# Kernel optimization log

Hardware: AMD Instinct MI355X
Metric: run time of the kernel (lower is better)

The kernel has to match this reference:

```python
import jax, jax.numpy as jnp
import numpy as np

NUM_EXPERTS = 8
M_TOTAL = 16384      # total routed tokens, sorted by expert
IN_FEATURES = 2048
OUT_FEATURES = 2048


def setup_inputs() -> dict:
    key = jax.random.key(0)
    k1, k2 = jax.random.split(key)
    x = jax.random.normal(k1, (M_TOTAL, IN_FEATURES), dtype=jnp.float32)
    # moe_fused_kaiming_uniform_: uniform(-sqrt(3*5/in), +sqrt(3*5/in))
    bound = float(np.sqrt(3.0 * 5.0 / IN_FEATURES))
    weight = jax.random.uniform(
        k2, (NUM_EXPERTS, OUT_FEATURES, IN_FEATURES),
        dtype=jnp.float32, minval=-bound, maxval=bound)
    # variable-size expert groups that sum exactly to M_TOTAL
    rng = np.random.default_rng(0)
    cuts = np.sort(rng.choice(np.arange(1, M_TOTAL), NUM_EXPERTS - 1, replace=False))
    m_sizes = np.diff(np.concatenate([[0], cuts, [M_TOTAL]])).astype(np.int32)
    return {"input": x, "weight": weight, "m_sizes": jnp.asarray(m_sizes)}


def reference(input, weight, m_sizes):
    """Grouped GEMM: rows of `input` are sorted by expert; the e-th contiguous
    block of m_sizes[e] rows is multiplied by weight[e].T ([out, in] -> x @ W_e^T)."""
    num_experts, out_features, _ = weight.shape
    m = input.shape[0]
    # per-token expert id from group sizes (jit-safe: fixed total length)
    expert_ids = jnp.repeat(jnp.arange(num_experts, dtype=jnp.int32), m_sizes,
                            total_repeat_length=m)  # [M]
    out = jnp.zeros((m, out_features), dtype=input.dtype)
    for e in range(num_experts):  # small fixed expert count
        mask = (expert_ids == e)[:, None]
        out = out + jnp.where(mask, input @ weight[e].T, jnp.zeros((), input.dtype))
    return out
```

## Files before the change

### kernel.cpp

```cpp
#include <hip/hip_runtime.h>
#include <hip/hip_bf16.h>

#define M_TOTAL 16384
#define KDIM 2048
#define NDIM 2048
#define NEXP 8
#define BM 256
#define BN 256
#define BK 32
#define NKT 64
#define MAX_ROW_TILES 71
#define NWG (MAX_ROW_TILES * 8)

typedef __attribute__((ext_vector_type(8))) __bf16 bf16x8;
typedef __attribute__((ext_vector_type(4))) float f32x4;

__device__ inline int minI(int a, int b) { return a < b ? a : b; }

__device__ inline bf16x8 cvt8(float4 a, float4 b) {
  bf16x8 r;
  r[0] = (__bf16)a.x; r[1] = (__bf16)a.y; r[2] = (__bf16)a.z; r[3] = (__bf16)a.w;
  r[4] = (__bf16)b.x; r[5] = (__bf16)b.y; r[6] = (__bf16)b.z; r[7] = (__bf16)b.w;
  return r;
}

__device__ inline void gload16(const void* g, void* l) {
  __builtin_amdgcn_global_load_lds(
      (const __attribute__((address_space(1))) void*)g,
      (__attribute__((address_space(3))) void*)l, 16, 0, 0);
}

__global__ __launch_bounds__(256) void cvt_both(
    const float* __restrict__ x, const float* __restrict__ w,
    bf16x8* __restrict__ xb, bf16x8* __restrict__ wb) {
  const int NX = (M_TOTAL * KDIM) / 8;
  const int NW = (NEXP * NDIM * KDIM) / 8;
  const int stride = gridDim.x * blockDim.x;
  for (int i = blockIdx.x * blockDim.x + threadIdx.x; i < NX + NW; i += stride) {
    const float4* src = (i < NX) ? ((const float4*)x + (size_t)i * 2)
                                 : ((const float4*)w + (size_t)(i - NX) * 2);
    float4 a = src[0], b = src[1];
    bf16x8 c = cvt8(a, b);
    if (i < NX) xb[i] = c; else wb[i - NX] = c;
  }
}

__global__ __launch_bounds__(512, 2) void moe_gemm_pipe(
    const __hip_bfloat16* __restrict__ xb, const __hip_bfloat16* __restrict__ wb,
    const int* __restrict__ ms, float* __restrict__ out) {
  __shared__ __align__(16) char lds[131072];

  const int orig = blockIdx.x;
  const int wg = (orig & 7) * MAX_ROW_TILES + (orig >> 3);
  const int bt = wg >> 3;
  const int ntile = wg & 7;

  int sizes[NEXP];
#pragma unroll
  for (int i = 0; i < NEXP; ++i) sizes[i] = ms[i];
  int e = 0, row0 = 0, rows = 0, acc_t = 0, start = 0;
  bool found = false;
#pragma unroll
  for (int i = 0; i < NEXP; ++i) {
    int nt = (sizes[i] + BM - 1) >> 8;
    if (!found && bt < acc_t + nt) {
      found = true; e = i;
      int tt = bt - acc_t;
      row0 = start + tt * BM;
      rows = minI(sizes[i] - tt * BM, BM);
    }
    acc_t += nt; start += sizes[i];
  }
  if (!found) return;

  const int tid = threadIdx.x;
  const int lane = tid & 63;
  const int wave = tid >> 6;
  const int wr = wave >> 2, wc = wave & 3;
  const int col0 = ntile * BN;

  const int rwh = wave * 16 + (lane >> 2);
  const int colel = (((lane & 3) ^ ((lane >> 3) & 3)) << 3);
  const __hip_bfloat16* aS0 = xb + (size_t)minI(row0 + rwh, M_TOTAL - 1) * KDIM + colel;
  const __hip_bfloat16* aS1 = xb + (size_t)minI(row0 + 128 + rwh, M_TOTAL - 1) * KDIM + colel;
  const __hip_bfloat16* wbase = wb + (size_t)e * NDIM * KDIM;
  const __hip_bfloat16* bS0 = wbase + (size_t)(col0 + rwh) * KDIM + colel;
  const __hip_bfloat16* bS1 = wbase + (size_t)(col0 + 128 + rwh) * KDIM + colel;
  char* stBase = lds + wave * 1024;

  const int fr = lane & 15, fc = lane >> 4;
  const int laneOff = fr * 64 + ((fc ^ ((fr >> 1) & 3)) << 4);
  const int aOff = wr * 8192 + laneOff;
  const int bOff = 16384 + wc * 4096 + laneOff;

  f32x4 acc[8][4];
  const f32x4 zero = {0.f, 0.f, 0.f, 0.f};
#pragma unroll
  for (int i = 0; i < 8; ++i)
#pragma unroll
    for (int j = 0; j < 4; ++j) acc[i][j] = zero;

  bf16x8 afL0[4], afL1[4], bv0[4], bv1[4], afH[4];

#define ISSUE_A(T) { char* b_ = stBase + ((T) & 3) * 32768; \
    gload16(aS0 + (size_t)(T) * BK, b_); gload16(aS1 + (size_t)(T) * BK, b_ + 8192); }
#define ISSUE_B(T) { char* b_ = stBase + ((T) & 3) * 32768 + 16384; \
    gload16(bS0 + (size_t)(T) * BK, b_); gload16(bS1 + (size_t)(T) * BK, b_ + 8192); }
#define DS_AFH(T) { const char* bA_ = lds + ((T) & 3) * 32768 + aOff + 4096; \
    _Pragma("unroll") for (int mt = 0; mt < 4; ++mt) \
      afH[mt] = *(const bf16x8*)(bA_ + mt * 1024); }
#define DS_NEXT(T, S) { const char* bb_ = lds + ((T) & 3) * 32768; \
    _Pragma("unroll") for (int mt = 0; mt < 4; ++mt) \
      afL##S[mt] = *(const bf16x8*)(bb_ + aOff + mt * 1024); \
    _Pragma("unroll") for (int nt = 0; nt < 4; ++nt) \
      bv##S[nt] = *(const bf16x8*)(bb_ + bOff + nt * 1024); }
#define MFMA_P0(S) { _Pragma("unroll") for (int mt = 0; mt < 4; ++mt) \
    _Pragma("unroll") for (int nt = 0; nt < 4; ++nt) \
      acc[mt][nt] = __builtin_amdgcn_mfma_f32_16x16x32_bf16( \
          afL##S[mt], bv##S[nt], acc[mt][nt], 0, 0, 0); }
#define MFMA_P1(S) { _Pragma("unroll") for (int mt = 0; mt < 4; ++mt) \
    _Pragma("unroll") for (int nt = 0; nt < 4; ++nt) \
      acc[mt + 4][nt] = __builtin_amdgcn_mfma_f32_16x16x32_bf16( \
          afH[mt], bv##S[nt], acc[mt + 4][nt], 0, 0, 0); }

#define TILE(T, S, SN, IA, IB, VMNSTR, NF) { \
    DS_AFH(T); \
    if (IA) ISSUE_A((T) + 3); \
    __builtin_amdgcn_s_setprio(1); MFMA_P0(S); __builtin_amdgcn_s_setprio(0); \
    asm volatile("s_waitcnt " VMNSTR ::: "memory"); \
    __builtin_amdgcn_s_barrier(); \
    if (NF) DS_NEXT((T) + 1, SN); \
    if (IB) ISSUE_B((T) + 3); \
    __builtin_amdgcn_s_setprio(1); MFMA_P1(S); __builtin_amdgcn_s_setprio(0); }

  ISSUE_A(0) ISSUE_B(0) ISSUE_A(1) ISSUE_B(1) ISSUE_A(2) ISSUE_B(2)
  asm volatile("s_waitcnt vmcnt(8)" ::: "memory");
  __builtin_amdgcn_s_barrier();
  DS_NEXT(0, 0);

  for (int tp = 0; tp < 30; ++tp) {
    const int t = tp * 2;
    TILE(t,     0, 1, true, true, "vmcnt(6)", true);
    TILE(t + 1, 1, 0, true, true, "vmcnt(6)", true);
  }
  TILE(60, 0, 1, true,  true,  "vmcnt(6)", true);
  TILE(61, 1, 0, false, false, "vmcnt(4)", true);
  TILE(62, 0, 1, false, false, "vmcnt(0)", true);
  TILE(63, 1, 0, false, false, "vmcnt(0)", false);

#undef TILE
#undef MFMA_P1
#undef MFMA_P0
#undef DS_NEXT
#undef DS_AFH
#undef ISSUE_B
#undef ISSUE_A

  const int er = (lane >> 4) * 4;
#pragma unroll
  for (int mt = 0; mt < 8; ++mt) {
#pragma unroll
    for (int j = 0; j < 4; ++j) {
      int r = wr * 128 + mt * 16 + er + j;
      if (r < rows) {
        float* op = out + (size_t)(row0 + r) * NDIM + col0 + wc * 64 + (lane & 15);
#pragma unroll
        for (int nt = 0; nt < 4; ++nt) op[nt * 16] = acc[mt][nt][j];
      }
    }
  }
}

__global__ __launch_bounds__(256) void moe_gemm_f32(
    const float* __restrict__ x, const float* __restrict__ w,
    const int* __restrict__ ms, float* __restrict__ out) {
  __shared__ __align__(16) char As[128 * 64 * 2];
  __shared__ __align__(16) char Bs[128 * 64 * 2];
  int sizes[NEXP];
#pragma unroll
  for (int i = 0; i < NEXP; ++i) sizes[i] = ms[i];
  const int bt = blockIdx.y;
  int e = 0, row0 = 0, rows = 0, acc_t = 0, start = 0;
  bool found = false;
#pragma unroll
  for (int i = 0; i < NEXP; ++i) {
    int nt = (sizes[i] + 127) >> 7;
    if (!found && bt < acc_t + nt) {
      found = true; e = i;
      int tt = bt - acc_t;
      row0 = start + tt * 128;
      rows = minI(sizes[i] - tt * 128, 128);
    }
    acc_t += nt; start += sizes[i];
  }
  if (!found) return;
  const int tid = threadIdx.x;
  const int lane = tid & 63;
  const int wave = tid >> 6;
  const int wm = wave >> 1, wn = wave & 1;
  const int col0 = blockIdx.x * 128;
  const float* wbase = w + (size_t)e * (size_t)NDIM * KDIM;
  const int sr = tid >> 1;
  const int sh = tid & 1;
  const float* aptr = x + (size_t)(row0 + sr) * KDIM + sh * 32;
  const float* bptr = wbase + (size_t)(col0 + sr) * KDIM + sh * 32;
  const bool aval = (sr < rows);
  f32x4 acc[4][4];
  const f32x4 zero = {0.f, 0.f, 0.f, 0.f};
#pragma unroll
  for (int i = 0; i < 4; ++i)
#pragma unroll
    for (int j = 0; j < 4; ++j) acc[i][j] = zero;
  for (int kb = 0; kb < KDIM / 64; ++kb) {
    {
      float4 v[8];
      if (aval) {
        const float4* p = (const float4*)(aptr + kb * 64);
#pragma unroll
        for (int j = 0; j < 8; ++j) v[j] = p[j];
      } else {
#pragma unroll
        for (int j = 0; j < 8; ++j) v[j] = make_float4(0.f, 0.f, 0.f, 0.f);
      }
#pragma unroll
      for (int j = 0; j < 4; ++j) {
        bf16x8 c = cvt8(v[2 * j], v[2 * j + 1]);
        int chunk = (sh * 4 + j) ^ (sr & 7);
        *(bf16x8*)(As + sr * 128 + chunk * 16) = c;
      }
    }
    {
      const float4* p = (const float4*)(bptr + kb * 64);
      float4 u[8];
#pragma unroll
      for (int j = 0; j < 8; ++j) u[j] = p[j];
#pragma unroll
      for (int j = 0; j < 4; ++j) {
        bf16x8 c = cvt8(u[2 * j], u[2 * j + 1]);
        int chunk = (sh * 4 + j) ^ (sr & 7);
        *(bf16x8*)(Bs + sr * 128 + chunk * 16) = c;
      }
    }
    __syncthreads();
#pragma unroll
    for (int ks = 0; ks < 2; ++ks) {
      bf16x8 afr[4], bfv[4];
#pragma unroll
      for (int mt = 0; mt < 4; ++mt) {
        int r = wm * 64 + mt * 16 + (lane & 15);
        int chunk = (ks * 4 + (lane >> 4)) ^ (r & 7);
        afr[mt] = *(const bf16x8*)(As + r * 128 + chunk * 16);
      }
#pragma unroll
      for (int nt = 0; nt < 4; ++nt) {
        int r = wn * 64 + nt * 16 + (lane & 15);
        int chunk = (ks * 4 + (lane >> 4)) ^ (r & 7);
        bfv[nt] = *(const bf16x8*)(Bs + r * 128 + chunk * 16);
      }
#pragma unroll
      for (int mt = 0; mt < 4; ++mt)
#pragma unroll
        for (int nt = 0; nt < 4; ++nt)
          acc[mt][nt] = __builtin_amdgcn_mfma_f32_16x16x32_bf16(
              afr[mt], bfv[nt], acc[mt][nt], 0, 0, 0);
    }
    __syncthreads();
  }
#pragma unroll
  for (int mt = 0; mt < 4; ++mt) {
#pragma unroll
    for (int j = 0; j < 4; ++j) {
      int r = wm * 64 + mt * 16 + (lane >> 4) * 4 + j;
      if (r < rows) {
        float* op = out + (size_t)(row0 + r) * NDIM + col0 + wn * 64 + (lane & 15);
#pragma unroll
        for (int nt = 0; nt < 4; ++nt) op[nt * 16] = acc[mt][nt][j];
      }
    }
  }
}

extern "C" void kernel_launch(void* const* d_in, const int* in_sizes, int n_in,
                              void* d_out, int out_size, void* d_ws, size_t ws_size,
                              hipStream_t stream) {
  const float* x = (const float*)d_in[0];
  const float* w = (const float*)d_in[1];
  const int* ms = (const int*)d_in[2];
  float* out = (float*)d_out;
  const size_t nx = (size_t)M_TOTAL * KDIM;
  const size_t nw = (size_t)NEXP * NDIM * KDIM;
  const size_t need = (nx + nw) * sizeof(__hip_bfloat16);
  if (ws_size >= need) {
    __hip_bfloat16* xb = (__hip_bfloat16*)d_ws;
    __hip_bfloat16* wb = xb + nx;
    cvt_both<<<2048, 256, 0, stream>>>(x, w, (bf16x8*)xb, (bf16x8*)wb);
    moe_gemm_pipe<<<dim3(NWG), dim3(512), 0, stream>>>(xb, wb, ms, out);
  } else {
    moe_gemm_f32<<<dim3(16, 135), dim3(256), 0, stream>>>(x, w, ms, out);
  }
}
```

Baseline: 243.5 us.

## Shrink GEMM tile to 256x128 with 3-stage LDS ring for more occupancy

```diff
diff --git a/kernel.cpp b/kernel.cpp
--- a/kernel.cpp
+++ b/kernel.cpp
@@ -6,11 +6,12 @@
 #define NDIM 2048
 #define NEXP 8
 #define BM 256
-#define BN 256
+#define BN 128
 #define BK 32
-#define NKT 64
-#define MAX_ROW_TILES 71
-#define NWG (MAX_ROW_TILES * 8)
+#define RT_MAX 71
+#define CT 16
+#define NWG (RT_MAX * CT)
+#define BUFB 24576
 
 typedef __attribute__((ext_vector_type(8))) __bf16 bf16x8;
 typedef __attribute__((ext_vector_type(4))) float f32x4;
@@ -45,15 +46,15 @@
   }
 }
 
-__global__ __launch_bounds__(512, 2) void moe_gemm_pipe(
+__global__ __launch_bounds__(512, 4) void moe_gemm_cores(
     const __hip_bfloat16* __restrict__ xb, const __hip_bfloat16* __restrict__ wb,
     const int* __restrict__ ms, float* __restrict__ out) {
-  __shared__ __align__(16) char lds[131072];
+  __shared__ __align__(16) char lds[3 * BUFB];
 
   const int orig = blockIdx.x;
-  const int wg = (orig & 7) * MAX_ROW_TILES + (orig >> 3);
-  const int bt = wg >> 3;
-  const int ntile = wg & 7;
+  const int wg = (orig & 7) * (NWG / 8) + (orig >> 3);
+  const int bt = wg >> 4;
+  const int ntile = wg & 15;
 
   int sizes[NEXP];
 #pragma unroll
@@ -76,7 +77,7 @@
   const int tid = threadIdx.x;
   const int lane = tid & 63;
   const int wave = tid >> 6;
-  const int wr = wave >> 2, wc = wave & 3;
+  const int wr = wave >> 1, wc = wave & 1;
   const int col0 = ntile * BN;
 
   const int rwh = wave * 16 + (lane >> 2);
@@ -84,84 +85,73 @@
   const __hip_bfloat16* aS0 = xb + (size_t)minI(row0 + rwh, M_TOTAL - 1) * KDIM + colel;
   const __hip_bfloat16* aS1 = xb + (size_t)minI(row0 + 128 + rwh, M_TOTAL - 1) * KDIM + colel;
   const __hip_bfloat16* wbase = wb + (size_t)e * NDIM * KDIM;
-  const __hip_bfloat16* bS0 = wbase + (size_t)(col0 + rwh) * KDIM + colel;
-  const __hip_bfloat16* bS1 = wbase + (size_t)(col0 + 128 + rwh) * KDIM + colel;
-  char* stBase = lds + wave * 1024;
+  const __hip_bfloat16* bS = wbase + (size_t)(col0 + rwh) * KDIM + colel;
 
   const int fr = lane & 15, fc = lane >> 4;
-  const int laneOff = fr * 64 + ((fc ^ ((fr >> 1) & 3)) << 4);
-  const int aOff = wr * 8192 + laneOff;
-  const int bOff = 16384 + wc * 4096 + laneOff;
-
-  f32x4 acc[8][4];
+  int offA[4], offB[4];
+#pragma unroll
+  for (int mt = 0; mt < 4; ++mt) {
+    int r = wr * 64 + mt * 16 + fr;
+    offA[mt] = r * 64 + ((fc ^ ((r >> 1) & 3)) << 4);
+  }
+#pragma unroll
+  for (int nt = 0; nt < 4; ++nt) {
+    int r = wc * 64 + nt * 16 + fr;
+    offB[nt] = 16384 + r * 64 + ((fc ^ ((r >> 1) & 3)) << 4);
+  }
+
+  f32x4 acc[4][4];
   const f32x4 zero = {0.f, 0.f, 0.f, 0.f};
 #pragma unroll
-  for (int i = 0; i < 8; ++i)
+  for (int i = 0; i < 4; ++i)
 #pragma unroll
     for (int j = 0; j < 4; ++j) acc[i][j] = zero;
 
-  bf16x8 afL0[4], afL1[4], bv0[4], bv1[4], afH[4];
-
-#define ISSUE_A(T) { char* b_ = stBase + ((T) & 3) * 32768; \
-    gload16(aS0 + (size_t)(T) * BK, b_); gload16(aS1 + (size_t)(T) * BK, b_ + 8192); }
-#define ISSUE_B(T) { char* b_ = stBase + ((T) & 3) * 32768 + 16384; \
-    gload16(bS0 + (size_t)(T) * BK, b_); gload16(bS1 + (size_t)(T) * BK, b_ + 8192); }
-#define DS_AFH(T) { const char* bA_ = lds + ((T) & 3) * 32768 + aOff + 4096; \
+#define ISSUE3(T, BI) { char* b_ = lds + (BI) * BUFB + wave * 1024; \
+    gload16(aS0 + (size_t)(T) * BK, b_); \
+    gload16(aS1 + (size_t)(T) * BK, b_ + 8192); \
+    gload16(bS + (size_t)(T) * BK, b_ + 16384); }
+
+#define TILE(T, BR, BI, VM, DOI) { \
+    asm volatile("s_waitcnt " VM ::: "memory"); \
+    __builtin_amdgcn_s_barrier(); \
+    if (DOI) ISSUE3((T) + 2, BI); \
+    const char* bb_ = lds + (BR) * BUFB; \
+    bf16x8 af[4], bv[4]; \
     _Pragma("unroll") for (int mt = 0; mt < 4; ++mt) \
-      afH[mt] = *(const bf16x8*)(bA_ + mt * 1024); }
-#define DS_NEXT(T, S) { const char* bb_ = lds + ((T) & 3) * 32768; \
+      af[mt] = *(const bf16x8*)(bb_ + offA[mt]); \
+    _Pragma("unroll") for (int nt = 0; nt < 4; ++nt) \
+      bv[nt] = *(const bf16x8*)(bb_ + offB[nt]); \
+    __builtin_amdgcn_s_setprio(1); \
     _Pragma("unroll") for (int mt = 0; mt < 4; ++mt) \
-      afL##S[mt] = *(const bf16x8*)(bb_ + aOff + mt * 1024); \
-    _Pragma("unroll") for (int nt = 0; nt < 4; ++nt) \
-      bv##S[nt] = *(const bf16x8*)(bb_ + bOff + nt * 1024); }
-#define MFMA_P0(S) { _Pragma("unroll") for (int mt = 0; mt < 4; ++mt) \
-    _Pragma("unroll") for (int nt = 0; nt < 4; ++nt) \
-      acc[mt][nt] = __builtin_amdgcn_mfma_f32_16x16x32_bf16( \
-          afL##S[mt], bv##S[nt], acc[mt][nt], 0, 0, 0); }
-#define MFMA_P1(S) { _Pragma("unroll") for (int mt = 0; mt < 4; ++mt) \
-    _Pragma("unroll") for (int nt = 0; nt < 4; ++nt) \
-      acc[mt + 4][nt] = __builtin_amdgcn_mfma_f32_16x16x32_bf16( \
-          afH[mt], bv##S[nt], acc[mt + 4][nt], 0, 0, 0); }
-
-#define TILE(T, S, SN, IA, IB, VMNSTR, NF) { \
-    DS_AFH(T); \
-    if (IA) ISSUE_A((T) + 3); \
-    __builtin_amdgcn_s_setprio(1); MFMA_P0(S); __builtin_amdgcn_s_setprio(0); \
-    asm volatile("s_waitcnt " VMNSTR ::: "memory"); \
-    __builtin_amdgcn_s_barrier(); \
-    if (NF) DS_NEXT((T) + 1, SN); \
-    if (IB) ISSUE_B((T) + 3); \
-    __builtin_amdgcn_s_setprio(1); MFMA_P1(S); __builtin_amdgcn_s_setprio(0); }
-
-  ISSUE_A(0) ISSUE_B(0) ISSUE_A(1) ISSUE_B(1) ISSUE_A(2) ISSUE_B(2)
-  asm volatile("s_waitcnt vmcnt(8)" ::: "memory");
-  __builtin_amdgcn_s_barrier();
-  DS_NEXT(0, 0);
-
-  for (int tp = 0; tp < 30; ++tp) {
-    const int t = tp * 2;
-    TILE(t,     0, 1, true, true, "vmcnt(6)", true);
-    TILE(t + 1, 1, 0, true, true, "vmcnt(6)", true);
-  }
-  TILE(60, 0, 1, true,  true,  "vmcnt(6)", true);
-  TILE(61, 1, 0, false, false, "vmcnt(4)", true);
-  TILE(62, 0, 1, false, false, "vmcnt(0)", true);
-  TILE(63, 1, 0, false, false, "vmcnt(0)", false);
+      _Pragma("unroll") for (int nt = 0; nt < 4; ++nt) \
+        acc[mt][nt] = __builtin_amdgcn_mfma_f32_16x16x32_bf16( \
+            af[mt], bv[nt], acc[mt][nt], 0, 0, 0); \
+    __builtin_amdgcn_s_setprio(0); }
+
+  ISSUE3(0, 0)
+  ISSUE3(1, 1)
+
+  for (int tp = 0; tp < 20; ++tp) {
+    const int t = tp * 3;
+    TILE(t,     0, 2, "vmcnt(3)", true);
+    TILE(t + 1, 1, 0, "vmcnt(3)", true);
+    TILE(t + 2, 2, 1, "vmcnt(3)", true);
+  }
+  TILE(60, 0, 2, "vmcnt(3)", true);
+  TILE(61, 1, 0, "vmcnt(3)", true);
+  TILE(62, 2, 1, "vmcnt(3)", false);
+  TILE(63, 0, 0, "vmcnt(0)", false);
 
 #undef TILE
-#undef MFMA_P1
-#undef MFMA_P0
-#undef DS_NEXT
-#undef DS_AFH
-#undef ISSUE_B
-#undef ISSUE_A
+#undef ISSUE3
 
   const int er = (lane >> 4) * 4;
 #pragma unroll
-  for (int mt = 0; mt < 8; ++mt) {
+  for (int mt = 0; mt < 4; ++mt) {
 #pragma unroll
     for (int j = 0; j < 4; ++j) {
-      int r = wr * 128 + mt * 16 + er + j;
+      int r = wr * 64 + mt * 16 + er + j;
       if (r < rows) {
         float* op = out + (size_t)(row0 + r) * NDIM + col0 + wc * 64 + (lane & 15);
 #pragma unroll
@@ -294,7 +284,7 @@
     __hip_bfloat16* xb = (__hip_bfloat16*)d_ws;
     __hip_bfloat16* wb = xb + nx;
     cvt_both<<<2048, 256, 0, stream>>>(x, w, (bf16x8*)xb, (bf16x8*)wb);
-    moe_gemm_pipe<<<dim3(NWG), dim3(512), 0, stream>>>(xb, wb, ms, out);
+    moe_gemm_cores<<<dim3(NWG), dim3(512), 0, stream>>>(xb, wb, ms, out);
   } else {
     moe_gemm_f32<<<dim3(16, 135), dim3(256), 0, stream>>>(x, w, ms, out);
   }
```

Measured after the change: 256.4 us. 5.3% more time.

## Restructure GEMM main loop into 8-phase double-buffered BK=64 pipeline

Applied to the files above, without the earlier changes.

```diff
diff --git a/kernel.cpp b/kernel.cpp
--- a/kernel.cpp
+++ b/kernel.cpp
@@ -7,8 +7,7 @@
 #define NEXP 8
 #define BM 256
 #define BN 256
-#define BK 32
-#define NKT 64
+#define BK 64
 #define MAX_ROW_TILES 71
 #define NWG (MAX_ROW_TILES * 8)
 
@@ -45,7 +44,7 @@
   }
 }
 
-__global__ __launch_bounds__(512, 2) void moe_gemm_pipe(
+__global__ __launch_bounds__(512, 2) void moe_gemm_8p(
     const __hip_bfloat16* __restrict__ xb, const __hip_bfloat16* __restrict__ wb,
     const int* __restrict__ ms, float* __restrict__ out) {
   __shared__ __align__(16) char lds[131072];
@@ -79,19 +78,23 @@
   const int wr = wave >> 2, wc = wave & 3;
   const int col0 = ntile * BN;
 
-  const int rwh = wave * 16 + (lane >> 2);
-  const int colel = (((lane & 3) ^ ((lane >> 3) & 3)) << 3);
-  const __hip_bfloat16* aS0 = xb + (size_t)minI(row0 + rwh, M_TOTAL - 1) * KDIM + colel;
-  const __hip_bfloat16* aS1 = xb + (size_t)minI(row0 + 128 + rwh, M_TOTAL - 1) * KDIM + colel;
+  const int urow = tid >> 3;
+  const int colel = (((tid & 7) ^ ((tid >> 3) & 7)) << 3);
   const __hip_bfloat16* wbase = wb + (size_t)e * NDIM * KDIM;
-  const __hip_bfloat16* bS0 = wbase + (size_t)(col0 + rwh) * KDIM + colel;
-  const __hip_bfloat16* bS1 = wbase + (size_t)(col0 + 128 + rwh) * KDIM + colel;
-  char* stBase = lds + wave * 1024;
+  const __hip_bfloat16* aP00 = xb + (size_t)minI(row0 +   0 + urow, M_TOTAL - 1) * KDIM + colel;
+  const __hip_bfloat16* aP01 = xb + (size_t)minI(row0 +  64 + urow, M_TOTAL - 1) * KDIM + colel;
+  const __hip_bfloat16* aP10 = xb + (size_t)minI(row0 + 128 + urow, M_TOTAL - 1) * KDIM + colel;
+  const __hip_bfloat16* aP11 = xb + (size_t)minI(row0 + 192 + urow, M_TOTAL - 1) * KDIM + colel;
+  const __hip_bfloat16* bP0 = wbase + (size_t)(col0 +   0 + urow) * KDIM + colel;
+  const __hip_bfloat16* bP1 = wbase + (size_t)(col0 +  64 + urow) * KDIM + colel;
+  const __hip_bfloat16* bP2 = wbase + (size_t)(col0 + 128 + urow) * KDIM + colel;
+  const __hip_bfloat16* bP3 = wbase + (size_t)(col0 + 192 + urow) * KDIM + colel;
 
   const int fr = lane & 15, fc = lane >> 4;
-  const int laneOff = fr * 64 + ((fc ^ ((fr >> 1) & 3)) << 4);
-  const int aOff = wr * 8192 + laneOff;
-  const int bOff = 16384 + wc * 4096 + laneOff;
+  const int swz0 = fr * 128 + (((fc) ^ (fr & 7)) << 4);
+  const int swz1 = fr * 128 + (((4 + fc) ^ (fr & 7)) << 4);
+  const int aBase = wr * 16384;
+  const int bBase = 32768 + (wc >> 1) * 16384 + (wc & 1) * 8192;
 
   f32x4 acc[8][4];
   const f32x4 zero = {0.f, 0.f, 0.f, 0.f};
@@ -100,61 +103,69 @@
 #pragma unroll
     for (int j = 0; j < 4; ++j) acc[i][j] = zero;
 
-  bf16x8 afL0[4], afL1[4], bv0[4], bv1[4], afH[4];
-
-#define ISSUE_A(T) { char* b_ = stBase + ((T) & 3) * 32768; \
-    gload16(aS0 + (size_t)(T) * BK, b_); gload16(aS1 + (size_t)(T) * BK, b_ + 8192); }
-#define ISSUE_B(T) { char* b_ = stBase + ((T) & 3) * 32768 + 16384; \
-    gload16(bS0 + (size_t)(T) * BK, b_); gload16(bS1 + (size_t)(T) * BK, b_ + 8192); }
-#define DS_AFH(T) { const char* bA_ = lds + ((T) & 3) * 32768 + aOff + 4096; \
+  bf16x8 af[4], bv[4];
+
+#define ST_A(D, H, L, KK) gload16(aP##H##L + (size_t)(KK) * BK, \
+    lds + (D) * 65536 + ((H) * 2 + (L)) * 8192 + wave * 1024);
+#define ST_B(D, Q, KK) gload16(bP##Q + (size_t)(KK) * BK, \
+    lds + (D) * 65536 + 32768 + (Q) * 8192 + wave * 1024);
+#define VM4 asm volatile("s_waitcnt vmcnt(4)" ::: "memory");
+#define VM2 asm volatile("s_waitcnt vmcnt(2)" ::: "memory");
+#define VM0 asm volatile("s_waitcnt vmcnt(0)" ::: "memory");
+
+#define PHASE(D, MH, SWZ, LOADB, STAGEBLK, WAITBLK) { \
     _Pragma("unroll") for (int mt = 0; mt < 4; ++mt) \
-      afH[mt] = *(const bf16x8*)(bA_ + mt * 1024); }
-#define DS_NEXT(T, S) { const char* bb_ = lds + ((T) & 3) * 32768; \
+      af[mt] = *(const bf16x8*)(lds + (D) * 65536 + aBase + ((MH) * 4 + mt) * 2048 + SWZ); \
+    if (LOADB) { _Pragma("unroll") for (int nt = 0; nt < 4; ++nt) \
+      bv[nt] = *(const bf16x8*)(lds + (D) * 65536 + bBase + nt * 2048 + SWZ); } \
+    STAGEBLK \
+    __builtin_amdgcn_s_barrier(); \
+    asm volatile("s_waitcnt lgkmcnt(0)" ::: "memory"); \
+    __builtin_amdgcn_s_setprio(1); \
     _Pragma("unroll") for (int mt = 0; mt < 4; ++mt) \
-      afL##S[mt] = *(const bf16x8*)(bb_ + aOff + mt * 1024); \
-    _Pragma("unroll") for (int nt = 0; nt < 4; ++nt) \
-      bv##S[nt] = *(const bf16x8*)(bb_ + bOff + nt * 1024); }
-#define MFMA_P0(S) { _Pragma("unroll") for (int mt = 0; mt < 4; ++mt) \
-    _Pragma("unroll") for (int nt = 0; nt < 4; ++nt) \
-      acc[mt][nt] = __builtin_amdgcn_mfma_f32_16x16x32_bf16( \
-          afL##S[mt], bv##S[nt], acc[mt][nt], 0, 0, 0); }
-#define MFMA_P1(S) { _Pragma("unroll") for (int mt = 0; mt < 4; ++mt) \
-    _Pragma("unroll") for (int nt = 0; nt < 4; ++nt) \
-      acc[mt + 4][nt] = __builtin_amdgcn_mfma_f32_16x16x32_bf16( \
-          afH[mt], bv##S[nt], acc[mt + 4][nt], 0, 0, 0); }
-
-#define TILE(T, S, SN, IA, IB, VMNSTR, NF) { \
-    DS_AFH(T); \
-    if (IA) ISSUE_A((T) + 3); \
-    __builtin_amdgcn_s_setprio(1); MFMA_P0(S); __builtin_amdgcn_s_setprio(0); \
-    asm volatile("s_waitcnt " VMNSTR ::: "memory"); \
+      _Pragma("unroll") for (int nt = 0; nt < 4; ++nt) \
+        acc[(MH) * 4 + mt][nt] = __builtin_amdgcn_mfma_f32_16x16x32_bf16( \
+            af[mt], bv[nt], acc[(MH) * 4 + mt][nt], 0, 0, 0); \
+    __builtin_amdgcn_s_setprio(0); \
+    WAITBLK \
+    asm volatile("" ::: "memory"); \
     __builtin_amdgcn_s_barrier(); \
-    if (NF) DS_NEXT((T) + 1, SN); \
-    if (IB) ISSUE_B((T) + 3); \
-    __builtin_amdgcn_s_setprio(1); MFMA_P1(S); __builtin_amdgcn_s_setprio(0); }
-
-  ISSUE_A(0) ISSUE_B(0) ISSUE_A(1) ISSUE_B(1) ISSUE_A(2) ISSUE_B(2)
-  asm volatile("s_waitcnt vmcnt(8)" ::: "memory");
+    asm volatile("" ::: "memory"); \
+  }
+
+  ST_B(0, 0, 0) ST_B(0, 1, 0) ST_B(0, 2, 0) ST_B(0, 3, 0)
+  ST_A(0, 0, 0, 0) ST_A(0, 1, 0, 0)
+  ST_A(0, 0, 1, 0) ST_A(0, 1, 1, 0)
+  ST_B(1, 0, 1) ST_B(1, 1, 1)
+  VM4
   __builtin_amdgcn_s_barrier();
-  DS_NEXT(0, 0);
-
-  for (int tp = 0; tp < 30; ++tp) {
-    const int t = tp * 2;
-    TILE(t,     0, 1, true, true, "vmcnt(6)", true);
-    TILE(t + 1, 1, 0, true, true, "vmcnt(6)", true);
-  }
-  TILE(60, 0, 1, true,  true,  "vmcnt(6)", true);
-  TILE(61, 1, 0, false, false, "vmcnt(4)", true);
-  TILE(62, 0, 1, false, false, "vmcnt(0)", true);
-  TILE(63, 1, 0, false, false, "vmcnt(0)", false);
-
-#undef TILE
-#undef MFMA_P1
-#undef MFMA_P0
-#undef DS_NEXT
-#undef DS_AFH
-#undef ISSUE_B
-#undef ISSUE_A
+
+  for (int i = 0; i < 15; ++i) {
+    const int t = 2 * i;
+    PHASE(0, 0, swz0, true,  { ST_B(1, 2, t + 1) ST_B(1, 3, t + 1) }, VM4)
+    PHASE(0, 1, swz0, false, { ST_A(1, 0, 0, t + 1) ST_A(1, 1, 0, t + 1) }, )
+    PHASE(0, 0, swz1, true,  { ST_A(1, 0, 1, t + 1) ST_A(1, 1, 1, t + 1) }, )
+    PHASE(0, 1, swz1, false, { ST_B(0, 0, t + 2) ST_B(0, 1, t + 2) }, VM4)
+    PHASE(1, 0, swz0, true,  { ST_B(0, 2, t + 2) ST_B(0, 3, t + 2) }, VM4)
+    PHASE(1, 1, swz0, false, { ST_A(0, 0, 0, t + 2) ST_A(0, 1, 0, t + 2) }, )
+    PHASE(1, 0, swz1, true,  { ST_A(0, 0, 1, t + 2) ST_A(0, 1, 1, t + 2) }, )
+    PHASE(1, 1, swz1, false, { ST_B(1, 0, t + 3) ST_B(1, 1, t + 3) }, VM4)
+  }
+  PHASE(0, 0, swz0, true,  { ST_B(1, 2, 31) ST_B(1, 3, 31) }, VM4)
+  PHASE(0, 1, swz0, false, { ST_A(1, 0, 0, 31) ST_A(1, 1, 0, 31) }, )
+  PHASE(0, 0, swz1, true,  { ST_A(1, 0, 1, 31) ST_A(1, 1, 1, 31) }, )
+  PHASE(0, 1, swz1, false, { }, VM2)
+  PHASE(1, 0, swz0, true,  { }, VM0)
+  PHASE(1, 1, swz0, false, { }, )
+  PHASE(1, 0, swz1, true,  { }, )
+  PHASE(1, 1, swz1, false, { }, )
+
+#undef PHASE
+#undef VM0
+#undef VM2
+#undef VM4
+#undef ST_B
+#undef ST_A
 
   const int er = (lane >> 4) * 4;
 #pragma unroll
@@ -294,7 +305,7 @@
     __hip_bfloat16* xb = (__hip_bfloat16*)d_ws;
     __hip_bfloat16* wb = xb + nx;
     cvt_both<<<2048, 256, 0, stream>>>(x, w, (bf16x8*)xb, (bf16x8*)wb);
-    moe_gemm_pipe<<<dim3(NWG), dim3(512), 0, stream>>>(xb, wb, ms, out);
+    moe_gemm_8p<<<dim3(NWG), dim3(512), 0, stream>>>(xb, wb, ms, out);
   } else {
     moe_gemm_f32<<<dim3(16, 135), dim3(256), 0, stream>>>(x, w, ms, out);
   }
```

Measured after the change: 239.1 us. About the same (-1.8%).

## Replace split-phase register prefetch pipeline with single-barrier 4-stage LDS ring

Applied to the files above, without the earlier changes.

```diff
diff --git a/kernel.cpp b/kernel.cpp
--- a/kernel.cpp
+++ b/kernel.cpp
@@ -8,7 +8,6 @@
 #define BM 256
 #define BN 256
 #define BK 32
-#define NKT 64
 #define MAX_ROW_TILES 71
 #define NWG (MAX_ROW_TILES * 8)
 
@@ -45,7 +44,7 @@
   }
 }
 
-__global__ __launch_bounds__(512, 2) void moe_gemm_pipe(
+__global__ __launch_bounds__(512, 2) void moe_gemm_sb(
     const __hip_bfloat16* __restrict__ xb, const __hip_bfloat16* __restrict__ wb,
     const int* __restrict__ ms, float* __restrict__ out) {
   __shared__ __align__(16) char lds[131072];
@@ -86,12 +85,11 @@
   const __hip_bfloat16* wbase = wb + (size_t)e * NDIM * KDIM;
   const __hip_bfloat16* bS0 = wbase + (size_t)(col0 + rwh) * KDIM + colel;
   const __hip_bfloat16* bS1 = wbase + (size_t)(col0 + 128 + rwh) * KDIM + colel;
-  char* stBase = lds + wave * 1024;
 
   const int fr = lane & 15, fc = lane >> 4;
   const int laneOff = fr * 64 + ((fc ^ ((fr >> 1) & 3)) << 4);
   const int aOff = wr * 8192 + laneOff;
-  const int bOff = 16384 + wc * 4096 + laneOff;
+  const int bOff = 16384 + (wc >> 1) * 8192 + (wc & 1) * 4096 + laneOff;
 
   f32x4 acc[8][4];
   const f32x4 zero = {0.f, 0.f, 0.f, 0.f};
@@ -100,61 +98,52 @@
 #pragma unroll
     for (int j = 0; j < 4; ++j) acc[i][j] = zero;
 
-  bf16x8 afL0[4], afL1[4], bv0[4], bv1[4], afH[4];
-
-#define ISSUE_A(T) { char* b_ = stBase + ((T) & 3) * 32768; \
-    gload16(aS0 + (size_t)(T) * BK, b_); gload16(aS1 + (size_t)(T) * BK, b_ + 8192); }
-#define ISSUE_B(T) { char* b_ = stBase + ((T) & 3) * 32768 + 16384; \
-    gload16(bS0 + (size_t)(T) * BK, b_); gload16(bS1 + (size_t)(T) * BK, b_ + 8192); }
-#define DS_AFH(T) { const char* bA_ = lds + ((T) & 3) * 32768 + aOff + 4096; \
-    _Pragma("unroll") for (int mt = 0; mt < 4; ++mt) \
-      afH[mt] = *(const bf16x8*)(bA_ + mt * 1024); }
-#define DS_NEXT(T, S) { const char* bb_ = lds + ((T) & 3) * 32768; \
-    _Pragma("unroll") for (int mt = 0; mt < 4; ++mt) \
-      afL##S[mt] = *(const bf16x8*)(bb_ + aOff + mt * 1024); \
+#define ST4(BI, T) { char* b_ = lds + (BI) * 32768 + wave * 1024; \
+    gload16(aS0 + (size_t)(T) * BK, b_); \
+    gload16(aS1 + (size_t)(T) * BK, b_ + 8192); \
+    gload16(bS0 + (size_t)(T) * BK, b_ + 16384); \
+    gload16(bS1 + (size_t)(T) * BK, b_ + 24576); }
+#define VM4 "vmcnt(4)"
+#define VM0 "vmcnt(0)"
+
+#define TILE(BI, T, DOST, VM) { \
+    asm volatile("s_waitcnt " VM ::: "memory"); \
+    __builtin_amdgcn_s_barrier(); \
+    asm volatile("" ::: "memory"); \
+    if (DOST) ST4(((BI) + 2) & 3, (T) + 2); \
+    const char* bb_ = lds + (BI) * 32768; \
+    bf16x8 af[8], bv[4]; \
+    _Pragma("unroll") for (int mt = 0; mt < 8; ++mt) \
+      af[mt] = *(const bf16x8*)(bb_ + aOff + mt * 1024); \
     _Pragma("unroll") for (int nt = 0; nt < 4; ++nt) \
-      bv##S[nt] = *(const bf16x8*)(bb_ + bOff + nt * 1024); }
-#define MFMA_P0(S) { _Pragma("unroll") for (int mt = 0; mt < 4; ++mt) \
-    _Pragma("unroll") for (int nt = 0; nt < 4; ++nt) \
-      acc[mt][nt] = __builtin_amdgcn_mfma_f32_16x16x32_bf16( \
-          afL##S[mt], bv##S[nt], acc[mt][nt], 0, 0, 0); }
-#define MFMA_P1(S) { _Pragma("unroll") for (int mt = 0; mt < 4; ++mt) \
-    _Pragma("unroll") for (int nt = 0; nt < 4; ++nt) \
-      acc[mt + 4][nt] = __builtin_amdgcn_mfma_f32_16x16x32_bf16( \
-          afH[mt], bv##S[nt], acc[mt + 4][nt], 0, 0, 0); }
-
-#define TILE(T, S, SN, IA, IB, VMNSTR, NF) { \
-    DS_AFH(T); \
-    if (IA) ISSUE_A((T) + 3); \
-    __builtin_amdgcn_s_setprio(1); MFMA_P0(S); __builtin_amdgcn_s_setprio(0); \
-    asm volatile("s_waitcnt " VMNSTR ::: "memory"); \
-    __builtin_amdgcn_s_barrier(); \
-    if (NF) DS_NEXT((T) + 1, SN); \
-    if (IB) ISSUE_B((T) + 3); \
-    __builtin_amdgcn_s_setprio(1); MFMA_P1(S); __builtin_amdgcn_s_setprio(0); }
-
-  ISSUE_A(0) ISSUE_B(0) ISSUE_A(1) ISSUE_B(1) ISSUE_A(2) ISSUE_B(2)
-  asm volatile("s_waitcnt vmcnt(8)" ::: "memory");
-  __builtin_amdgcn_s_barrier();
-  DS_NEXT(0, 0);
-
-  for (int tp = 0; tp < 30; ++tp) {
-    const int t = tp * 2;
-    TILE(t,     0, 1, true, true, "vmcnt(6)", true);
-    TILE(t + 1, 1, 0, true, true, "vmcnt(6)", true);
-  }
-  TILE(60, 0, 1, true,  true,  "vmcnt(6)", true);
-  TILE(61, 1, 0, false, false, "vmcnt(4)", true);
-  TILE(62, 0, 1, false, false, "vmcnt(0)", true);
-  TILE(63, 1, 0, false, false, "vmcnt(0)", false);
+      bv[nt] = *(const bf16x8*)(bb_ + bOff + nt * 1024); \
+    __builtin_amdgcn_s_setprio(1); \
+    _Pragma("unroll") for (int mt = 0; mt < 8; ++mt) \
+      _Pragma("unroll") for (int nt = 0; nt < 4; ++nt) \
+        acc[mt][nt] = __builtin_amdgcn_mfma_f32_16x16x32_bf16( \
+            af[mt], bv[nt], acc[mt][nt], 0, 0, 0); \
+    __builtin_amdgcn_s_setprio(0); \
+  }
+
+  ST4(0, 0)
+  ST4(1, 1)
+
+  for (int i = 0; i < 15; ++i) {
+    const int t = 4 * i;
+    TILE(0, t,     true, VM4)
+    TILE(1, t + 1, true, VM4)
+    TILE(2, t + 2, true, VM4)
+    TILE(3, t + 3, true, VM4)
+  }
+  TILE(0, 60, true,  VM4)
+  TILE(1, 61, true,  VM4)
+  TILE(2, 62, false, VM4)
+  TILE(3, 63, false, VM0)
 
 #undef TILE
-#undef MFMA_P1
-#undef MFMA_P0
-#undef DS_NEXT
-#undef DS_AFH
-#undef ISSUE_B
-#undef ISSUE_A
+#undef VM0
+#undef VM4
+#undef ST4
 
   const int er = (lane >> 4) * 4;
 #pragma unroll
@@ -294,7 +283,7 @@
     __hip_bfloat16* xb = (__hip_bfloat16*)d_ws;
     __hip_bfloat16* wb = xb + nx;
     cvt_both<<<2048, 256, 0, stream>>>(x, w, (bf16x8*)xb, (bf16x8*)wb);
-    moe_gemm_pipe<<<dim3(NWG), dim3(512), 0, stream>>>(xb, wb, ms, out);
+    moe_gemm_sb<<<dim3(NWG), dim3(512), 0, stream>>>(xb, wb, ms, out);
   } else {
     moe_gemm_f32<<<dim3(16, 135), dim3(256), 0, stream>>>(x, w, ms, out);
   }
```

Result: slower. 248.4 us (+2.0%).
